# Performance work log

Hardware: AMD Instinct MI355X
Metric: run time of the kernel (lower is better)

## Reference

```python
import jax, jax.numpy as jnp
import numpy as np

B, N, D, C, H = 8, 2048, 768, 2048, 3072
ROPE_BASE = 10000.0


def rms_norm(x, scale, eps=1e-6):
    x32 = x.astype(jnp.float32)
    normed = x32 * jax.lax.rsqrt(jnp.mean(x32 * x32, axis=-1, keepdims=True) + eps)
    return normed.astype(x.dtype) * scale


def apply_rope(x, pos):
    # x: [..., T, D], pos: [..., T] int. Half-split (llama-style) rotary embedding.
    half = x.shape[-1] // 2
    inv_freq = 1.0 / (ROPE_BASE ** (jnp.arange(half, dtype=jnp.float32) / half))
    ang = pos.astype(jnp.float32)[..., None] * inv_freq  # [..., T, half]
    cos, sin = jnp.cos(ang), jnp.sin(ang)
    x1, x2 = x[..., :half], x[..., half:]
    return jnp.concatenate([x1 * cos - x2 * sin, x1 * sin + x2 * cos], axis=-1)


def setup_inputs() -> dict:
    key = jax.random.key(0)
    ks = jax.random.split(key, 12)
    inp = {
        "latents": jax.random.normal(ks[0], (B, N, D), dtype=jnp.float32),
        "tau": jnp.float32(1.0),
        "residual_scaling": jnp.float32(1.0),
        "gumbel_noise_scale": jnp.float32(0.5),
        "positions": jnp.sort(jax.random.randint(ks[1], (B, max(N, C)), 0, 2048), axis=-1),
        # learned parameters (torch Linear weights stored [out, in])
        "codebook": jax.random.normal(ks[2], (C, D), dtype=jnp.float32),
        "norm_context_scale": jnp.ones((D,), jnp.float32),
        "norm_queries_scale": jnp.ones((D,), jnp.float32),
        "norm_ff_scale": jnp.ones((D,), jnp.float32),
        "Wq": jax.random.normal(ks[3], (D, D), jnp.float32) / np.sqrt(D),
        "Wk": jax.random.normal(ks[4], (D, D), jnp.float32) / np.sqrt(D),
        "Wv": jax.random.normal(ks[5], (D, D), jnp.float32) / np.sqrt(D),
        "bv": jnp.zeros((D,), jnp.float32),
        "Wc": jax.random.normal(ks[6], (D, D), jnp.float32) / np.sqrt(D),
        "W1": jax.random.normal(ks[7], (H, D), jnp.float32) / np.sqrt(D),
        "W2": jax.random.normal(ks[8], (D, H), jnp.float32) / np.sqrt(H),
        "W3": jax.random.normal(ks[9], (H, D), jnp.float32) / np.sqrt(D),
    }
    return inp


def reference(latents, tau, residual_scaling, gumbel_noise_scale, positions,
              codebook, norm_context_scale, norm_queries_scale, norm_ff_scale,
              Wq, Wk, Wv, bv, Wc, W1, W2, W3):
    scale = jnp.sqrt(jnp.float32(D))
    normed_context = rms_norm(codebook, norm_context_scale)        # [C, D]
    normed_queries = rms_norm(latents, norm_queries_scale)         # [B, N, D]

    q = jnp.einsum('bnd,ed->bne', normed_queries, Wq)              # [B, N, D]
    k = normed_context @ Wk.T                                      # [C, D]
    v = normed_context @ Wv.T + bv                                 # [C, D]

    q = apply_rope(q, positions[:, :N])                            # [B, N, D]
    k = apply_rope(jnp.broadcast_to(k, (B, C, D)), positions[:, :C])  # [B, C, D]

    log_alpha = jnp.einsum('bnd,bcd->bnc', q, k) / scale           # [B, N, C]

    u = jax.random.uniform(jax.random.key(42), log_alpha.shape, dtype=jnp.float32)
    gumbel = -jnp.log(-jnp.log(u + 1e-10) + 1e-10)
    log_alpha_tau = (log_alpha + gumbel_noise_scale * gumbel) / tau
    z = jax.nn.softmax(log_alpha_tau, axis=-1)                     # [B, N, C]

    attn = jnp.einsum('bnc,cd->bnd', z, v)                         # [B, N, D]
    y = jnp.einsum('bnd,ed->bne', attn, Wc)
    attn_output = residual_scaling * latents + y

    h = rms_norm(attn_output, norm_ff_scale)
    ff = jnp.einsum('bnh,dh->bnd', jax.nn.silu(jnp.einsum('bnd,hd->bnh', h, W1)) * jnp.einsum('bnd,hd->bnh', h, W3), W2)
    codebook_output = attn_output + ff
    return (codebook_output, log_alpha, log_alpha_tau, z)
```

## Files before the change

kernel.cpp:

```cpp
#include <hip/hip_runtime.h>
#include <cstdint>
#include <cstddef>


typedef __bf16 bf16_t;
typedef __bf16 bf16x8 __attribute__((ext_vector_type(8)));
typedef float  f32x4  __attribute__((ext_vector_type(4)));

#define B_    8
#define N_    2048
#define D_    768
#define C_    2048
#define H_    3072
#define NROWS 16384

#define WQ_OFF 0
#define WK_OFF 589824
#define WV_OFF 1179648
#define WC_OFF 1769472
#define W1_OFF 2359296
#define W3_OFF 4718592
#define W2_OFF 7077888
#define WTOT   9437184

#define WS_W     0ull
#define WS_TRIG  18874368ull
#define WS_VCT   25165824ull
#define WS_NC    28311552ull
#define WS_NQ    31457280ull
#define WS_Z     56623104ull
#define WS_H     28311552ull
#define WS_G     157286400ull
#define WS_VB    257949696ull

#define DO_CB    0ull
#define DO_LA    50331648ull
#define DO_LAT   184549376ull
#define DO_Z     318767104ull
#define DO_QBASE 184549376ull
#define DO_KBASE (184549376ull + 50331648ull)
// ... 20 lines not shown
__device__ __forceinline__ void tf_round(uint32_t& x0, uint32_t& x1, int r) {
  x0 += x1; x1 = rotl32(x1, r); x1 ^= x0;
}
__device__ __forceinline__ uint2 threefry2x32(uint32_t k0, uint32_t k1,
                                              uint32_t x0, uint32_t x1) {
  const uint32_t k2 = k0 ^ k1 ^ 0x1BD11BDAu;
  x0 += k0; x1 += k1;
  tf_round(x0,x1,13); tf_round(x0,x1,15); tf_round(x0,x1,26); tf_round(x0,x1,6);
  x0 += k1; x1 += k2 + 1u;
  tf_round(x0,x1,17); tf_round(x0,x1,29); tf_round(x0,x1,16); tf_round(x0,x1,24);
  x0 += k2; x1 += k0 + 2u;
  tf_round(x0,x1,13); tf_round(x0,x1,15); tf_round(x0,x1,26); tf_round(x0,x1,6);
  x0 += k0; x1 += k1 + 3u;
  tf_round(x0,x1,17); tf_round(x0,x1,29); tf_round(x0,x1,16); tf_round(x0,x1,24);
  x0 += k1; x1 += k2 + 4u;
  tf_round(x0,x1,13); tf_round(x0,x1,15); tf_round(x0,x1,26); tf_round(x0,x1,6);
  x0 += k2; x1 += k0 + 5u;
  return make_uint2(x0, x1);
}

#define SWZ(o) ((o) ^ ((((o) >> 7) & 3) << 4))

#define PHASE_MFMA_OPEN() do { \
    block_sync(); \
    asm volatile("s_waitcnt lgkmcnt(0)" ::: "memory"); \
    __builtin_amdgcn_sched_barrier(0); \
    __builtin_amdgcn_s_setprio(1); \
  } while (0)
#define PHASE_MFMA_CLOSE() do { \
    __builtin_amdgcn_s_setprio(0); \
    __builtin_amdgcn_sched_barrier(0); \
  } while (0)

template <int EPI>
__global__ __launch_bounds__(512, 2) void gemm8p(
    const bf16_t* __restrict__ A, const bf16_t* __restrict__ B,
    void* outp, const void* auxp, const float* sptr,
    int M, int N, int K, long sA, long sB, long sO)
{
  __shared__ bf16_t As[2][2][8192];
  __shared__ bf16_t Bs[2][2][8192];
  const int tid  = threadIdx.x;
  const int lane = tid & 63;
  const int wid  = tid >> 6;
  const int wm = wid >> 2, wn = wid & 3;
  const int fr = lane & 15, fg = lane >> 4;
  const int bz = blockIdx.z;
  const bf16_t* Ab = A + (size_t)bz * (size_t)sA;
  const bf16_t* Bb = B + (size_t)bz * (size_t)sB;
  const int tm = blockIdx.y * 256;
  const int tn = blockIdx.x * 256;
  const int nt = K >> 6;

  const bf16_t *srcA0, *srcA1, *srcB0, *srcB1;
  {
    const int d0 = wid * 1024 + lane * 16;
    const int p0 = SWZ(d0);
    srcA0 = Ab + (size_t)(tm + (p0 >> 6)) * K + ((p0 & 63) >> 1);
    srcB0 = Bb + (size_t)(tn + (p0 >> 6)) * K + ((p0 & 63) >> 1);
    const int d1 = 8192 + wid * 1024 + lane * 16;
    const int p1 = SWZ(d1);
    srcA1 = Ab + (size_t)(tm + (p1 >> 6)) * K + ((p1 & 63) >> 1);
    srcB1 = Bb + (size_t)(tn + (p1 >> 6)) * K + ((p1 & 63) >> 1);
  }
  bf16_t* dstA = &As[0][0][0] + wid * 512;
  bf16_t* dstB = &Bs[0][0][0] + wid * 512;

  int olB[4], olA[2][4];
  #pragma unroll
  for (int n = 0; n < 4; ++n) {
    const int o = ((wn * 64 + n * 16 + fr) << 6) + (fg << 4);
    olB[n] = SWZ(o);
  }
  #pragma unroll
  for (int mh = 0; mh < 2; ++mh)
    #pragma unroll
    for (int j = 0; j < 4; ++j) {
      const int o = ((wm * 128 + mh * 64 + j * 16 + fr) << 6) + (fg << 4);
      olA[mh][j] = SWZ(o);
    }

#define STG_A(tile_, kk_) do { \
    const size_t ko_ = (size_t)(tile_) * 64 + (size_t)(kk_) * 32; \
    bf16_t* db_ = dstA + (((tile_) & 1) ? 16384 : 0) + ((kk_) ? 8192 : 0); \
    gl_lds16(srcA0 + ko_, db_); \
    gl_lds16(srcA1 + ko_, db_ + 4096); \
  } while (0)
#define STG_B(tile_, kk_) do { \
    const size_t ko_ = (size_t)(tile_) * 64 + (size_t)(kk_) * 32; \
    bf16_t* db_ = dstB + (((tile_) & 1) ? 16384 : 0) + ((kk_) ? 8192 : 0); \
    gl_lds16(srcB0 + ko_, db_); \
    gl_lds16(srcB1 + ko_, db_ + 4096); \
  } while (0)

  f32x4 acc[8][4] = {};

  STG_A(0, 0); STG_B(0, 0); STG_A(0, 1); STG_B(0, 1);
  STG_B(1, 0); STG_A(1, 0); STG_B(1, 1);
  asm volatile("s_waitcnt vmcnt(6)" ::: "memory");
  block_sync();

  for (int t = 0; t < nt; ++t) {
    const int s = t & 1;
    bf16x8 bfr[4];
    #pragma unroll
    for (int q = 0; q < 4; ++q) {
      const int kk = q >> 1, mh = q & 1;
      if (q == 0)      { if (t + 1 < nt) STG_A(t + 1, 1); }
      else if (q == 1) { if (t + 2 < nt) STG_B(t + 2, 0); }
      else if (q == 2) { if (t + 2 < nt) STG_A(t + 2, 0); }
      else             { if (t + 2 < nt) STG_B(t + 2, 1); }
      if (mh == 0) {
        const char* Bbase = (const char*)&Bs[s][kk][0];
        #pragma unroll
        for (int n = 0; n < 4; ++n)
          bfr[n] = *(const bf16x8*)(Bbase + olB[n]);
      }
      const char* Abase = (const char*)&As[s][kk][0];
      bf16x8 af[4];
      #pragma unroll
      for (int j = 0; j < 4; ++j)
        af[j] = *(const bf16x8*)(Abase + olA[mh][j]);
      PHASE_MFMA_OPEN();
      #pragma unroll
      for (int j = 0; j < 4; ++j) {
        #pragma unroll
        for (int n = 0; n < 4; ++n)
          acc[mh * 4 + j][n] =
            __builtin_amdgcn_mfma_f32_16x16x32_bf16(af[j], bfr[n], acc[mh * 4 + j][n], 0, 0, 0);
      }
      PHASE_MFMA_CLOSE();
      if (q == 3) asm volatile("s_waitcnt vmcnt(6)" ::: "memory");
      block_sync();
    }
  }
#undef STG_A
#undef STG_B

  #pragma unroll
  for (int m = 0; m < 8; ++m) {
    const int rb = wm * 128 + m * 16 + fg * 4;
    #pragma unroll
    for (int n = 0; n < 4; ++n) {
      const int cg = tn + wn * 64 + n * 16 + fr;
      #pragma unroll
      for (int j = 0; j < 4; ++j) {
        const int r = tm + rb + j;
        const float v = acc[m][n][j];
        const size_t idx = (size_t)r * N + cg;
        if (EPI == 1) {
          ((float*)outp)[(size_t)bz * sO + idx] = v * 0.03608439182435161f;
        } else {
          ((float*)outp)[(size_t)bz * sO + idx] = v;
        }
      }
    }
  }
}

template <int EPI>
__global__ __launch_bounds__(512, 2) void gemm_n384(
    const bf16_t* __restrict__ A, const bf16_t* __restrict__ B,
    void* outp, const void* auxp, const float* sptr, int K)
{
  __shared__ bf16_t As[2][2][4096];
  __shared__ bf16_t Bs[2][2][12288];
  const int tid  = threadIdx.x;
  const int lane = tid & 63;
  const int wid  = tid >> 6;
  const int wm = wid >> 2, wn = wid & 3;
  const int fr = lane & 15, fg = lane >> 4;
  const int tm = blockIdx.y * 128;
  const int tn = blockIdx.x * 384;
  const int nt = K >> 6;

  const bf16_t *srcA, *srcB0, *srcB1, *srcB2;
  {
    const int d = wid * 1024 + lane * 16;
    const int p = SWZ(d);
    srcA = A + (size_t)(tm + (p >> 6)) * K + ((p & 63) >> 1);
    srcB0 = B + (size_t)(tn + (p >> 6)) * K + ((p & 63) >> 1);
    const int d1 = 8192 + d, p1 = SWZ(d1);
    srcB1 = B + (size_t)(tn + (p1 >> 6)) * K + ((p1 & 63) >> 1);
    const int d2 = 16384 + d, p2 = SWZ(d2);
    srcB2 = B + (size_t)(tn + (p2 >> 6)) * K + ((p2 & 63) >> 1);
  }
  bf16_t* dstA = &As[0][0][0] + wid * 512;
  bf16_t* dstB = &Bs[0][0][0] + wid * 512;

  int olB[6], olA[2][2];
  #pragma unroll
  for (int n = 0; n < 6; ++n) {
    const int o = ((wn * 96 + n * 16 + fr) << 6) + (fg << 4);
    olB[n] = SWZ(o);
  }
  #pragma unroll
  for (int mh = 0; mh < 2; ++mh)
    #pragma unroll
    for (int j = 0; j < 2; ++j) {
      const int o = ((wm * 64 + (mh * 2 + j) * 16 + fr) << 6) + (fg << 4);
      olA[mh][j] = SWZ(o);
    }

#define STG_A(tile_, kk_) do { \
    const size_t ko_ = (size_t)(tile_) * 64 + (size_t)(kk_) * 32; \
    gl_lds16(srcA + ko_, dstA + (((tile_) & 1) ? 8192 : 0) + ((kk_) ? 4096 : 0)); \
  } while (0)
#define STG_B(tile_, kk_) do { \
    const size_t ko_ = (size_t)(tile_) * 64 + (size_t)(kk_) * 32; \
    bf16_t* db_ = dstB + (((tile_) & 1) ? 24576 : 0) + ((kk_) ? 12288 : 0); \
    gl_lds16(srcB0 + ko_, db_); \
    gl_lds16(srcB1 + ko_, db_ + 4096); \
    gl_lds16(srcB2 + ko_, db_ + 8192); \
  } while (0)

  f32x4 acc[4][6] = {};

  STG_A(0, 0); STG_B(0, 0); STG_A(0, 1); STG_B(0, 1);
  STG_B(1, 0); STG_A(1, 0); STG_B(1, 1);
  asm volatile("s_waitcnt vmcnt(7)" ::: "memory");
  block_sync();

  for (int t = 0; t < nt; ++t) {
    const int s = t & 1;
    bf16x8 bfr[6];
    #pragma unroll
    for (int q = 0; q < 4; ++q) {
      const int kk = q >> 1, mh = q & 1;
      if (q == 0)      { if (t + 1 < nt) STG_A(t + 1, 1); }
      else if (q == 1) { if (t + 2 < nt) STG_B(t + 2, 0); }
      else if (q == 2) { if (t + 2 < nt) STG_A(t + 2, 0); }
      else             { if (t + 2 < nt) STG_B(t + 2, 1); }
      if (mh == 0) {
        const char* Bbase = (const char*)&Bs[s][kk][0];
        #pragma unroll
        for (int n = 0; n < 6; ++n)
          bfr[n] = *(const bf16x8*)(Bbase + olB[n]);
      }
      const char* Abase = (const char*)&As[s][kk][0];
      bf16x8 af[2];
      #pragma unroll
      for (int j = 0; j < 2; ++j)
        af[j] = *(const bf16x8*)(Abase + olA[mh][j]);
      PHASE_MFMA_OPEN();
      #pragma unroll
      for (int j = 0; j < 2; ++j) {
        #pragma unroll
        for (int n = 0; n < 6; ++n)
          acc[mh * 2 + j][n] =
            __builtin_amdgcn_mfma_f32_16x16x32_bf16(af[j], bfr[n], acc[mh * 2 + j][n], 0, 0, 0);
      }
      PHASE_MFMA_CLOSE();
      if (q == 3) asm volatile("s_waitcnt vmcnt(7)" ::: "memory");
      block_sync();
    }
  }
#undef STG_A
#undef STG_B

  const float sval = (EPI == 5) ? sptr[0] : 0.0f;
  #pragma unroll
  for (int m = 0; m < 4; ++m) {
    const int rb = wm * 64 + m * 16 + fg * 4;
    #pragma unroll
    for (int n = 0; n < 6; ++n) {
      const int cg = tn + wn * 96 + n * 16 + fr;
      #pragma unroll
      for (int j = 0; j < 4; ++j) {
        const int r = tm + rb + j;
        const float v = acc[m][n][j];
        const size_t idx = (size_t)r * 768 + cg;
        if (EPI == 2) {
          ((bf16_t*)outp)[idx] = (bf16_t)v;
        } else if (EPI == 5) {
          ((float*)outp)[idx] = sval * ((const float*)auxp)[idx] + v;
        } else {
          ((float*)outp)[idx] = ((const float*)auxp)[idx] + v;
        }
      }
    }
  }
}

__global__ __launch_bounds__(512, 2) void gemm_ff13(
    const bf16_t* __restrict__ A, const bf16_t* __restrict__ B1,
    const bf16_t* __restrict__ B3, bf16_t* __restrict__ G, int K)
{
  __shared__ bf16_t As[2][2][8192];
  __shared__ bf16_t B1s[2][2][4096];
  __shared__ bf16_t B3s[2][2][4096];
  const int tid  = threadIdx.x;
  const int lane = tid & 63;
  const int wid  = tid >> 6;
  const int wm = wid >> 2, wn = wid & 3;
  const int fr = lane & 15, fg = lane >> 4;
  const int tm = blockIdx.y * 256;
  const int tn = blockIdx.x * 128;
  const int nt = K >> 6;

  const bf16_t *srcA0, *srcA1, *srcB1p, *srcB3p;
  {
    const int d0 = wid * 1024 + lane * 16;
    const int p0 = SWZ(d0);
    srcA0 = A + (size_t)(tm + (p0 >> 6)) * K + ((p0 & 63) >> 1);
    srcB1p = B1 + (size_t)(tn + (p0 >> 6)) * K + ((p0 & 63) >> 1);
    srcB3p = B3 + (size_t)(tn + (p0 >> 6)) * K + ((p0 & 63) >> 1);
    const int d1 = 8192 + d0, p1 = SWZ(d1);
    srcA1 = A + (size_t)(tm + (p1 >> 6)) * K + ((p1 & 63) >> 1);
  }
  bf16_t* dstA  = &As[0][0][0]  + wid * 512;
  bf16_t* dstB1 = &B1s[0][0][0] + wid * 512;
  bf16_t* dstB3 = &B3s[0][0][0] + wid * 512;

  int olB[2], olA[2][4];
  #pragma unroll
  for (int n = 0; n < 2; ++n) {
    const int o = ((wn * 32 + n * 16 + fr) << 6) + (fg << 4);
    olB[n] = SWZ(o);
  }
  #pragma unroll
  for (int mh = 0; mh < 2; ++mh)
    #pragma unroll
    for (int j = 0; j < 4; ++j) {
      const int o = ((wm * 128 + mh * 64 + j * 16 + fr) << 6) + (fg << 4);
      olA[mh][j] = SWZ(o);
    }

#define STG_A(tile_, kk_) do { \
    const size_t ko_ = (size_t)(tile_) * 64 + (size_t)(kk_) * 32; \
    bf16_t* db_ = dstA + (((tile_) & 1) ? 16384 : 0) + ((kk_) ? 8192 : 0); \
    gl_lds16(srcA0 + ko_, db_); \
    gl_lds16(srcA1 + ko_, db_ + 4096); \
  } while (0)
#define STG_B(tile_, kk_) do { \
    const size_t ko_ = (size_t)(tile_) * 64 + (size_t)(kk_) * 32; \
    const int ro_ = (((tile_) & 1) ? 8192 : 0) + ((kk_) ? 4096 : 0); \
    gl_lds16(srcB1p + ko_, dstB1 + ro_); \
    gl_lds16(srcB3p + ko_, dstB3 + ro_); \
  } while (0)

  f32x4 acc1[8][2] = {};
  f32x4 acc3[8][2] = {};

  STG_A(0, 0); STG_B(0, 0); STG_A(0, 1); STG_B(0, 1);
  STG_B(1, 0); STG_A(1, 0); STG_B(1, 1);
  asm volatile("s_waitcnt vmcnt(6)" ::: "memory");
  block_sync();

  for (int t = 0; t < nt; ++t) {
    const int s = t & 1;
    bf16x8 b1r[2], b3r[2];
    #pragma unroll
    for (int q = 0; q < 4; ++q) {
      const int kk = q >> 1, mh = q & 1;
      if (q == 0)      { if (t + 1 < nt) STG_A(t + 1, 1); }
      else if (q == 1) { if (t + 2 < nt) STG_B(t + 2, 0); }
      else if (q == 2) { if (t + 2 < nt) STG_A(t + 2, 0); }
      else             { if (t + 2 < nt) STG_B(t + 2, 1); }
      if (mh == 0) {
        const char* B1base = (const char*)&B1s[s][kk][0];
        const char* B3base = (const char*)&B3s[s][kk][0];
        #pragma unroll
        for (int n = 0; n < 2; ++n) {
          b1r[n] = *(const bf16x8*)(B1base + olB[n]);
          b3r[n] = *(const bf16x8*)(B3base + olB[n]);
        }
      }
      const char* Abase = (const char*)&As[s][kk][0];
      bf16x8 af[4];
      #pragma unroll
      for (int j = 0; j < 4; ++j)
        af[j] = *(const bf16x8*)(Abase + olA[mh][j]);
      PHASE_MFMA_OPEN();
      #pragma unroll
      for (int j = 0; j < 4; ++j) {
        #pragma unroll
        for (int n = 0; n < 2; ++n) {
          acc1[mh * 4 + j][n] =
            __builtin_amdgcn_mfma_f32_16x16x32_bf16(af[j], b1r[n], acc1[mh * 4 + j][n], 0, 0, 0);
          acc3[mh * 4 + j][n] =
            __builtin_amdgcn_mfma_f32_16x16x32_bf16(af[j], b3r[n], acc3[mh * 4 + j][n], 0, 0, 0);
        }
      }
      PHASE_MFMA_CLOSE();
      if (q == 3) asm volatile("s_waitcnt vmcnt(6)" ::: "memory");
      block_sync();
    }
  }
#undef STG_A
#undef STG_B

  #pragma unroll
  for (int m = 0; m < 8; ++m) {
    const int rb = wm * 128 + m * 16 + fg * 4;
    #pragma unroll
    for (int n = 0; n < 2; ++n) {
      const int cg = tn + wn * 32 + n * 16 + fr;
      #pragma unroll
      for (int j = 0; j < 4; ++j) {
        const int r = tm + rb + j;
        const float f1 = acc1[m][n][j];
        const float f3 = acc3[m][n][j];
        const float sg = f1 / (1.0f + expf(-f1));
        G[(size_t)r * 3072 + cg] = (bf16_t)(sg * f3);
      }
    }
  }
}

template <int EPI>
__global__ __launch_bounds__(256) void gemm_bt(
    const bf16_t* __restrict__ A, const bf16_t* __restrict__ B,
    void* outp, const void* auxp, int M, int N, int K)
{
  __shared__ bf16_t Asl[128 * 64];
  __shared__ bf16_t Bsl[128 * 64];
  const int tid  = threadIdx.x;
  const int lane = tid & 63;
  const int wid  = tid >> 6;
  const int tm = blockIdx.y * 128;
  const int tn = blockIdx.x * 128;
  const int row0 = (wid & 1) * 64;
  const int col0 = (wid >> 1) * 64;
  const int fr = lane & 15;
  const int fg = lane >> 4;

  f32x4 acc[4][4] = {};

  for (int k0 = 0; k0 < K; k0 += 64) {
    #pragma unroll
    for (int i = 0; i < 4; ++i) {
      const int ebase = (i * 4 + wid) * 512;
      const int e0 = ebase + lane * 8;
      const int r  = e0 >> 6;
      const int c  = e0 & 63;
      gl_lds16(A + (size_t)(tm + r) * K + (k0 + c), &Asl[ebase]);
      gl_lds16(B + (size_t)(tn + r) * K + (k0 + c), &Bsl[ebase]);
    }
    __syncthreads();

    #pragma unroll
    for (int kk = 0; kk < 2; ++kk) {
      bf16x8 af[4], bfv[4];
      #pragma unroll
      for (int m = 0; m < 4; ++m)
        af[m] = *(const bf16x8*)&Asl[(row0 + m * 16 + fr) * 64 + kk * 32 + fg * 8];
      #pragma unroll
      for (int n = 0; n < 4; ++n)
        bfv[n] = *(const bf16x8*)&Bsl[(col0 + n * 16 + fr) * 64 + kk * 32 + fg * 8];
      #pragma unroll
      for (int m = 0; m < 4; ++m) {
        #pragma unroll
        for (int n = 0; n < 4; ++n)
          acc[m][n] = __builtin_amdgcn_mfma_f32_16x16x32_bf16(af[m], bfv[n], acc[m][n], 0, 0, 0);
      }
    }
    __syncthreads();
  }

  #pragma unroll
  for (int m = 0; m < 4; ++m) {
    const int rb = row0 + m * 16 + fg * 4;
    #pragma unroll
    for (int n = 0; n < 4; ++n) {
      const int cg = tn + col0 + n * 16 + fr;
      #pragma unroll
      for (int j = 0; j < 4; ++j) {
        const int r = tm + rb + j;
        const float v = acc[m][n][j];
        if (EPI == 2) {
          ((bf16_t*)outp)[(size_t)r * N + cg] = (bf16_t)v;
        } else if (EPI == 7) {
          ((bf16_t*)outp)[(size_t)cg * M + r] = (bf16_t)v;
        } else if (EPI == 8) {
          ((bf16_t*)outp)[(size_t)r * N + cg] = (bf16_t)(v + ((const float*)auxp)[cg]);
        }
      }
    }
  }
}

__global__ __launch_bounds__(256) void rms_rows(const float* __restrict__ x,
                                                const float* __restrict__ scale,
                                                bf16_t* __restrict__ out)
{
  const int row = blockIdx.x, t = threadIdx.x;
  const float* xr = x + (size_t)row * 768;
  const float v0 = xr[t], v1 = xr[t + 256], v2 = xr[t + 512];
  float ss = v0 * v0 + v1 * v1 + v2 * v2;
  #pragma unroll
  for (int m = 32; m; m >>= 1) ss += __shfl_xor(ss, m);
  __shared__ float red[4];
  if ((t & 63) == 0) red[t >> 6] = ss;
  __syncthreads();
  const float tot = red[0] + red[1] + red[2] + red[3];
  const float inv = rsqrtf(tot / 768.0f + 1e-6f);
  bf16_t* orow = out + (size_t)row * 768;
  orow[t]       = (bf16_t)(v0 * inv * scale[t]);
  orow[t + 256] = (bf16_t)(v1 * inv * scale[t + 256]);
  orow[t + 512] = (bf16_t)(v2 * inv * scale[t + 512]);
}

__global__ __launch_bounds__(128) void trig_fill(float* __restrict__ trig)
{
  const int p = blockIdx.x, t = threadIdx.x;
  #pragma unroll
  for (int j = 0; j < 3; ++j) {
    const int i = t + j * 128;
    const float invf = expf(-(float)i * (9.210340371976184f / 384.0f));
    const float ang  = (float)p * invf;
    trig[(size_t)p * 768 + i]       = cosf(ang);
    trig[(size_t)p * 768 + 384 + i] = sinf(ang);
  }
}

__global__ __launch_bounds__(128) void rope_rows(const bf16_t* __restrict__ src,
                                                 const int* __restrict__ pos,
                                                 const float* __restrict__ trig,
                                                 bf16_t* __restrict__ dst, int mask)
{
  const int row = blockIdx.x, t = threadIdx.x;
  const int p = pos[row];
  const bf16_t* s = src + (size_t)(row & mask) * 768;
  const float* tr = trig + (size_t)p * 768;
  bf16_t* d = dst + (size_t)row * 768;
  #pragma unroll
  for (int j = 0; j < 3; ++j) {
    const int i = t + j * 128;
    const float x1 = (float)s[i], x2 = (float)s[i + 384];
    const float c = tr[i], sn = tr[i + 384];
    d[i]       = (bf16_t)(x1 * c - x2 * sn);
    d[i + 384] = (bf16_t)(x1 * sn + x2 * c);
  }
}

__global__ __launch_bounds__(256) void softmax_g(const float* __restrict__ la,
                                                 float* __restrict__ lat,
                                                 float* __restrict__ z,
                                                 bf16_t* __restrict__ zb,
                                                 const float* __restrict__ taup,
                                                 const float* __restrict__ gnsp)
{
  const int row = blockIdx.x, t = threadIdx.x;
  const float tau = taup[0], gns = gnsp[0];
  const float* lar = la + (size_t)row * 2048;
  float* latr = lat + (size_t)row * 2048;
  float* zr   = z   + (size_t)row * 2048;
  bf16_t* zbr = zb  + (size_t)row * 2048;
  const uint32_t base = (uint32_t)row * 2048u;

  float vals[8];
  float mx = -3.0e38f;
  #pragma unroll
  for (int j = 0; j < 8; ++j) {
    const int c = t + j * 256;
    const uint32_t flat = base + (uint32_t)c;
    const uint2 rr = threefry2x32(0u, 42u, 0u, flat);
    const uint32_t bits = rr.x ^ rr.y;
    const float u = __uint_as_float((bits >> 9) | 0x3f800000u) - 1.0f;
    const float gum = -logf(-logf(u + 1e-10f) + 1e-10f);
    const float v = (lar[c] + gns * gum) / tau;
    vals[j] = v;
    latr[c] = v;
    mx = fmaxf(mx, v);
  }
  #pragma unroll
  for (int m = 32; m; m >>= 1) mx = fmaxf(mx, __shfl_xor(mx, m));
  __shared__ float redm[4];
  if ((t & 63) == 0) redm[t >> 6] = mx;
  __syncthreads();
  mx = fmaxf(fmaxf(redm[0], redm[1]), fmaxf(redm[2], redm[3]));

  float sum = 0.0f;
  #pragma unroll
  for (int j = 0; j < 8; ++j) { vals[j] = expf(vals[j] - mx); sum += vals[j]; }
  #pragma unroll
  for (int m = 32; m; m >>= 1) sum += __shfl_xor(sum, m);
  __shared__ float reds[4];
  if ((t & 63) == 0) reds[t >> 6] = sum;
  __syncthreads();
  sum = reds[0] + reds[1] + reds[2] + reds[3];

  #pragma unroll
  for (int j = 0; j < 8; ++j) {
    const int c = t + j * 256;
    const float zz = vals[j] / sum;
    zr[c]  = zz;
    zbr[c] = (bf16_t)zz;
  }
}

__global__ __launch_bounds__(256) void convert_w(
    const float* __restrict__ wq, const float* __restrict__ wk,
    const float* __restrict__ wv, const float* __restrict__ wc,
    const float* __restrict__ w1, const float* __restrict__ w3,
    const float* __restrict__ w2, bf16_t* __restrict__ dst)
{
  const int idx = blockIdx.x * 256 + threadIdx.x;
  const float* src; int off;
  if      (idx < 589824)  { src = wq; off = 0; }
  else if (idx < 1179648) { src = wk; off = 589824; }
  else if (idx < 1769472) { src = wv; off = 1179648; }
  else if (idx < 2359296) { src = wc; off = 1769472; }
  else if (idx < 4718592) { src = w1; off = 2359296; }
  else if (idx < 7077888) { src = w3; off = 4718592; }
  else                    { src = w2; off = 7077888; }
  dst[idx] = (bf16_t)src[idx - off];
}

extern "C" void kernel_launch(void* const* d_in, const int* in_sizes, int n_in,
                              void* d_out, int out_size, void* d_ws, size_t ws_size,
                              hipStream_t stream)
{
  (void)in_sizes; (void)n_in; (void)out_size; (void)ws_size;
  const float* latents   = (const float*)d_in[0];
  const float* taup      = (const float*)d_in[1];
  const float* rsp       = (const float*)d_in[2];
  const float* gnsp      = (const float*)d_in[3];
  const int*   positions = (const int*)d_in[4];
// ... 3 lines not shown
  const float* nfs       = (const float*)d_in[8];
  const float* Wq = (const float*)d_in[9];
  const float* Wk = (const float*)d_in[10];
  const float* Wv = (const float*)d_in[11];
  const float* bv = (const float*)d_in[12];
  const float* Wc = (const float*)d_in[13];
  const float* W1 = (const float*)d_in[14];
  const float* W2 = (const float*)d_in[15];
  const float* W3 = (const float*)d_in[16];

  char* ws = (char*)d_ws;
  char* ob = (char*)d_out;

  bf16_t* wbf  = (bf16_t*)(ws + WS_W);
  float*  trig = (float*)(ws + WS_TRIG);
  bf16_t* vcT  = (bf16_t*)(ws + WS_VCT);
  bf16_t* nc   = (bf16_t*)(ws + WS_NC);
  bf16_t* nq   = (bf16_t*)(ws + WS_NQ);
  bf16_t* zbuf = (bf16_t*)(ws + WS_Z);
  bf16_t* hbuf = (bf16_t*)(ws + WS_H);
  bf16_t* gbuf = (bf16_t*)(ws + WS_G);
  bf16_t* vbuf = (bf16_t*)(ws + WS_VB);

  float*  out_cb  = (float*)(ob + DO_CB);
  float*  out_la  = (float*)(ob + DO_LA);
  float*  out_lat = (float*)(ob + DO_LAT);
  float*  out_z   = (float*)(ob + DO_Z);
  bf16_t* qbase   = (bf16_t*)(ob + DO_QBASE);
  bf16_t* kbase   = (bf16_t*)(ob + DO_KBASE);
  bf16_t* qrope   = (bf16_t*)(ob + DO_QROPE);
  bf16_t* krope   = (bf16_t*)(ob + DO_KROPE);

  convert_w<<<dim3(WTOT / 256), dim3(256), 0, stream>>>(Wq, Wk, Wv, Wc, W1, W3, W2, wbf);
  rms_rows<<<dim3(C_),    dim3(256), 0, stream>>>(codebook, ncs, nc);
  rms_rows<<<dim3(NROWS), dim3(256), 0, stream>>>(latents,  nqs, nq);
  trig_fill<<<dim3(2048), dim3(128), 0, stream>>>(trig);

  gemm_bt<2><<<dim3(6, 16), dim3(256), 0, stream>>>(nc,   wbf + WK_OFF, kbase, nullptr, C_, D_, D_);
  gemm_bt<8><<<dim3(6, 16), dim3(256), 0, stream>>>(nc,   wbf + WV_OFF, vbuf,  bv,      C_, D_, D_);
  gemm_bt<7><<<dim3(6, 16), dim3(256), 0, stream>>>(vbuf, wbf + WC_OFF, vcT,   nullptr, C_, D_, D_);
  gemm_n384<2><<<dim3(2, 128), dim3(512), 0, stream>>>(nq, wbf + WQ_OFF, qbase, nullptr, nullptr, D_);

  rope_rows<<<dim3(NROWS), dim3(128), 0, stream>>>(qbase, positions, trig, qrope, 0x7fffffff);
  rope_rows<<<dim3(NROWS), dim3(128), 0, stream>>>(kbase, positions, trig, krope, 2047);

  gemm8p<1><<<dim3(8, 8, 8), dim3(512), 0, stream>>>(qrope, krope, out_la, nullptr, nullptr,
                                                     N_, C_, D_, (long)N_ * D_, (long)C_ * D_, (long)N_ * C_);

  softmax_g<<<dim3(NROWS), dim3(256), 0, stream>>>(out_la, out_lat, out_z, zbuf, taup, gnsp);

  gemm_n384<5><<<dim3(2, 128), dim3(512), 0, stream>>>(zbuf, vcT, out_cb, latents, rsp, C_);

  rms_rows<<<dim3(NROWS), dim3(256), 0, stream>>>(out_cb, nfs, hbuf);

  gemm_ff13<<<dim3(24, 64), dim3(512), 0, stream>>>(hbuf, wbf + W1_OFF, wbf + W3_OFF, gbuf, D_);
  gemm_n384<6><<<dim3(2, 128), dim3(512), 0, stream>>>(gbuf, wbf + W2_OFF, out_cb, out_cb, nullptr, H_);
}
```

Measured before the change: 852.6 us.

## Switch GEMMs to 32x32x16 MFMA, fuse RoPE launches, use fast math intrinsics

Moves the three main GEMM kernels from 16x16x32 to 32x32x16 bf16 MFMA tiles, which changes the LDS fragment offsets, the accumulator layout and the epilogue row mapping. The larger MFMA tiles cut the number of LDS fragment reads per FLOP. It also merges the Q and K RoPE launches into one grid, and uses __expf/__logf plus a reciprocal multiply in the softmax and SiLU paths. Fast intrinsics carry small accuracy differences, and the epilogue stores become less coalesced in their row pattern.

```diff
diff --git a/kernel.cpp b/kernel.cpp
--- a/kernel.cpp
+++ b/kernel.cpp
@@ -6,6 +6,7 @@
 typedef __bf16 bf16_t;
 typedef __bf16 bf16x8 __attribute__((ext_vector_type(8)));
 typedef float  f32x4  __attribute__((ext_vector_type(4)));
+typedef float  f32x16 __attribute__((ext_vector_type(16)));
 
 #define B_    8
 #define N_    2048
@@ -92,6 +93,8 @@
     __builtin_amdgcn_sched_barrier(0); \
   } while (0)
 
+#define ROWMAP32(rg, kg) (((rg) & 3) + 8 * ((rg) >> 2) + 4 * (kg))
+
 template <int EPI>
 __global__ __launch_bounds__(512, 2) void gemm8p(
     const bf16_t* __restrict__ A, const bf16_t* __restrict__ B,
@@ -104,7 +107,7 @@
   const int lane = tid & 63;
   const int wid  = tid >> 6;
   const int wm = wid >> 2, wn = wid & 3;
-  const int fr = lane & 15, fg = lane >> 4;
+  const int l31 = lane & 31, kg = lane >> 5;
   const int bz = blockIdx.z;
   const bf16_t* Ab = A + (size_t)bz * (size_t)sA;
   const bf16_t* Bb = B + (size_t)bz * (size_t)sB;
@@ -126,18 +129,20 @@
   bf16_t* dstA = &As[0][0][0] + wid * 512;
   bf16_t* dstB = &Bs[0][0][0] + wid * 512;
 
-  int olB[4], olA[2][4];
-  #pragma unroll
-  for (int n = 0; n < 4; ++n) {
-    const int o = ((wn * 64 + n * 16 + fr) << 6) + (fg << 4);
-    olB[n] = SWZ(o);
-  }
-  #pragma unroll
-  for (int mh = 0; mh < 2; ++mh)
-    #pragma unroll
-    for (int j = 0; j < 4; ++j) {
-      const int o = ((wm * 128 + mh * 64 + j * 16 + fr) << 6) + (fg << 4);
-      olA[mh][j] = SWZ(o);
+  int olA[4][2], olB[2][2];
+  #pragma unroll
+  for (int mb = 0; mb < 4; ++mb)
+    #pragma unroll
+    for (int u = 0; u < 2; ++u) {
+      const int o = ((wm * 128 + mb * 32 + l31) << 6) + u * 32 + (kg << 4);
+      olA[mb][u] = SWZ(o);
+    }
+  #pragma unroll
+  for (int nb = 0; nb < 2; ++nb)
+    #pragma unroll
+    for (int u = 0; u < 2; ++u) {
+      const int o = ((wn * 64 + nb * 32 + l31) << 6) + u * 32 + (kg << 4);
+      olB[nb][u] = SWZ(o);
     }
 
 #define STG_A(tile_, kk_) do { \
@@ -153,7 +158,7 @@
     gl_lds16(srcB1 + ko_, db_ + 4096); \
   } while (0)
 
-  f32x4 acc[8][4] = {};
+  f32x16 acc[4][2] = {};
 
   STG_A(0, 0); STG_B(0, 0); STG_A(0, 1); STG_B(0, 1);
   STG_B(1, 0); STG_A(1, 0); STG_B(1, 1);
@@ -162,7 +167,7 @@
 
   for (int t = 0; t < nt; ++t) {
     const int s = t & 1;
-    bf16x8 bfr[4];
+    bf16x8 bfr[2][2];
     #pragma unroll
     for (int q = 0; q < 4; ++q) {
       const int kk = q >> 1, mh = q & 1;
@@ -173,22 +178,27 @@
       if (mh == 0) {
         const char* Bbase = (const char*)&Bs[s][kk][0];
         #pragma unroll
-        for (int n = 0; n < 4; ++n)
-          bfr[n] = *(const bf16x8*)(Bbase + olB[n]);
+        for (int nb = 0; nb < 2; ++nb)
+          #pragma unroll
+          for (int u = 0; u < 2; ++u)
+            bfr[nb][u] = *(const bf16x8*)(Bbase + olB[nb][u]);
       }
       const char* Abase = (const char*)&As[s][kk][0];
-      bf16x8 af[4];
-      #pragma unroll
-      for (int j = 0; j < 4; ++j)
-        af[j] = *(const bf16x8*)(Abase + olA[mh][j]);
+      bf16x8 af[2][2];
+      #pragma unroll
+      for (int j = 0; j < 2; ++j)
+        #pragma unroll
+        for (int u = 0; u < 2; ++u)
+          af[j][u] = *(const bf16x8*)(Abase + olA[mh * 2 + j][u]);
       PHASE_MFMA_OPEN();
       #pragma unroll
-      for (int j = 0; j < 4; ++j) {
-        #pragma unroll
-        for (int n = 0; n < 4; ++n)
-          acc[mh * 4 + j][n] =
-            __builtin_amdgcn_mfma_f32_16x16x32_bf16(af[j], bfr[n], acc[mh * 4 + j][n], 0, 0, 0);
-      }
+      for (int u = 0; u < 2; ++u)
+        #pragma unroll
+        for (int j = 0; j < 2; ++j)
+          #pragma unroll
+          for (int nb = 0; nb < 2; ++nb)
+            acc[mh * 2 + j][nb] =
+              __builtin_amdgcn_mfma_f32_32x32x16_bf16(af[j][u], bfr[nb][u], acc[mh * 2 + j][nb], 0, 0, 0);
       PHASE_MFMA_CLOSE();
       if (q == 3) asm volatile("s_waitcnt vmcnt(6)" ::: "memory");
       block_sync();
@@ -198,15 +208,14 @@
 #undef STG_B
 
   #pragma unroll
-  for (int m = 0; m < 8; ++m) {
-    const int rb = wm * 128 + m * 16 + fg * 4;
-    #pragma unroll
-    for (int n = 0; n < 4; ++n) {
-      const int cg = tn + wn * 64 + n * 16 + fr;
-      #pragma unroll
-      for (int j = 0; j < 4; ++j) {
-        const int r = tm + rb + j;
-        const float v = acc[m][n][j];
+  for (int mb = 0; mb < 4; ++mb) {
+    #pragma unroll
+    for (int nb = 0; nb < 2; ++nb) {
+      const int cg = tn + wn * 64 + nb * 32 + l31;
+      #pragma unroll
+      for (int rg = 0; rg < 16; ++rg) {
+        const int r = tm + wm * 128 + mb * 32 + ROWMAP32(rg, kg);
+        const float v = acc[mb][nb][rg];
         const size_t idx = (size_t)r * N + cg;
         if (EPI == 1) {
           ((float*)outp)[(size_t)bz * sO + idx] = v * 0.03608439182435161f;
@@ -229,7 +238,7 @@
   const int lane = tid & 63;
   const int wid  = tid >> 6;
   const int wm = wid >> 2, wn = wid & 3;
-  const int fr = lane & 15, fg = lane >> 4;
+  const int l31 = lane & 31, kg = lane >> 5;
   const int tm = blockIdx.y * 128;
   const int tn = blockIdx.x * 384;
   const int nt = K >> 6;
@@ -248,18 +257,20 @@
   bf16_t* dstA = &As[0][0][0] + wid * 512;
   bf16_t* dstB = &Bs[0][0][0] + wid * 512;
 
-  int olB[6], olA[2][2];
-  #pragma unroll
-  for (int n = 0; n < 6; ++n) {
-    const int o = ((wn * 96 + n * 16 + fr) << 6) + (fg << 4);
-    olB[n] = SWZ(o);
-  }
-  #pragma unroll
-  for (int mh = 0; mh < 2; ++mh)
-    #pragma unroll
-    for (int j = 0; j < 2; ++j) {
-      const int o = ((wm * 64 + (mh * 2 + j) * 16 + fr) << 6) + (fg << 4);
-      olA[mh][j] = SWZ(o);
+  int olA[2][2], olB[3][2];
+  #pragma unroll
+  for (int mb = 0; mb < 2; ++mb)
+    #pragma unroll
+    for (int u = 0; u < 2; ++u) {
+      const int o = ((wm * 64 + mb * 32 + l31) << 6) + u * 32 + (kg << 4);
+      olA[mb][u] = SWZ(o);
+    }
+  #pragma unroll
+  for (int nb = 0; nb < 3; ++nb)
+    #pragma unroll
+    for (int u = 0; u < 2; ++u) {
+      const int o = ((wn * 96 + nb * 32 + l31) << 6) + u * 32 + (kg << 4);
+      olB[nb][u] = SWZ(o);
     }
 
 #define STG_A(tile_, kk_) do { \
@@ -274,7 +285,7 @@
     gl_lds16(srcB2 + ko_, db_ + 8192); \
   } while (0)
 
-  f32x4 acc[4][6] = {};
+  f32x16 acc[2][3] = {};
 
   STG_A(0, 0); STG_B(0, 0); STG_A(0, 1); STG_B(0, 1);
   STG_B(1, 0); STG_A(1, 0); STG_B(1, 1);
@@ -283,7 +294,7 @@
 
   for (int t = 0; t < nt; ++t) {
     const int s = t & 1;
-    bf16x8 bfr[6];
+    bf16x8 bfr[3][2];
     #pragma unroll
     for (int q = 0; q < 4; ++q) {
       const int kk = q >> 1, mh = q & 1;
@@ -294,22 +305,23 @@
       if (mh == 0) {
         const char* Bbase = (const char*)&Bs[s][kk][0];
         #pragma unroll
-        for (int n = 0; n < 6; ++n)
-          bfr[n] = *(const bf16x8*)(Bbase + olB[n]);
+        for (int nb = 0; nb < 3; ++nb)
+          #pragma unroll
+          for (int u = 0; u < 2; ++u)
+            bfr[nb][u] = *(const bf16x8*)(Bbase + olB[nb][u]);
       }
       const char* Abase = (const char*)&As[s][kk][0];
       bf16x8 af[2];
       #pragma unroll
-      for (int j = 0; j < 2; ++j)
-        af[j] = *(const bf16x8*)(Abase + olA[mh][j]);
+      for (int u = 0; u < 2; ++u)
+        af[u] = *(const bf16x8*)(Abase + olA[mh][u]);
       PHASE_MFMA_OPEN();
       #pragma unroll
-      for (int j = 0; j < 2; ++j) {
-        #pragma unroll
-        for (int n = 0; n < 6; ++n)
-          acc[mh * 2 + j][n] =
-            __builtin_amdgcn_mfma_f32_16x16x32_bf16(af[j], bfr[n], acc[mh * 2 + j][n], 0, 0, 0);
-      }
+      for (int u = 0; u < 2; ++u)
+        #pragma unroll
+        for (int nb = 0; nb < 3; ++nb)
+          acc[mh][nb] =
+            __builtin_amdgcn_mfma_f32_32x32x16_bf16(af[u], bfr[nb][u], acc[mh][nb], 0, 0, 0);
       PHASE_MFMA_CLOSE();
       if (q == 3) asm volatile("s_waitcnt vmcnt(7)" ::: "memory");
       block_sync();
@@ -320,15 +332,14 @@
 
   const float sval = (EPI == 5) ? sptr[0] : 0.0f;
   #pragma unroll
-  for (int m = 0; m < 4; ++m) {
-    const int rb = wm * 64 + m * 16 + fg * 4;
-    #pragma unroll
-    for (int n = 0; n < 6; ++n) {
-      const int cg = tn + wn * 96 + n * 16 + fr;
-      #pragma unroll
-      for (int j = 0; j < 4; ++j) {
-        const int r = tm + rb + j;
-        const float v = acc[m][n][j];
+  for (int mb = 0; mb < 2; ++mb) {
+    #pragma unroll
+    for (int nb = 0; nb < 3; ++nb) {
+      const int cg = tn + wn * 96 + nb * 32 + l31;
+      #pragma unroll
+      for (int rg = 0; rg < 16; ++rg) {
+        const int r = tm + wm * 64 + mb * 32 + ROWMAP32(rg, kg);
+        const float v = acc[mb][nb][rg];
         const size_t idx = (size_t)r * 768 + cg;
         if (EPI == 2) {
           ((bf16_t*)outp)[idx] = (bf16_t)v;
@@ -353,7 +364,7 @@
   const int lane = tid & 63;
   const int wid  = tid >> 6;
   const int wm = wid >> 2, wn = wid & 3;
-  const int fr = lane & 15, fg = lane >> 4;
+  const int l31 = lane & 31, kg = lane >> 5;
   const int tm = blockIdx.y * 256;
   const int tn = blockIdx.x * 128;
   const int nt = K >> 6;
@@ -372,19 +383,19 @@
   bf16_t* dstB1 = &B1s[0][0][0] + wid * 512;
   bf16_t* dstB3 = &B3s[0][0][0] + wid * 512;
 
-  int olB[2], olA[2][4];
-  #pragma unroll
-  for (int n = 0; n < 2; ++n) {
-    const int o = ((wn * 32 + n * 16 + fr) << 6) + (fg << 4);
-    olB[n] = SWZ(o);
-  }
-  #pragma unroll
-  for (int mh = 0; mh < 2; ++mh)
-    #pragma unroll
-    for (int j = 0; j < 4; ++j) {
-      const int o = ((wm * 128 + mh * 64 + j * 16 + fr) << 6) + (fg << 4);
-      olA[mh][j] = SWZ(o);
-    }
+  int olA[4][2], olB[2];
+  #pragma unroll
+  for (int mb = 0; mb < 4; ++mb)
+    #pragma unroll
+    for (int u = 0; u < 2; ++u) {
+      const int o = ((wm * 128 + mb * 32 + l31) << 6) + u * 32 + (kg << 4);
+      olA[mb][u] = SWZ(o);
+    }
+  #pragma unroll
+  for (int u = 0; u < 2; ++u) {
+    const int o = ((wn * 32 + l31) << 6) + u * 32 + (kg << 4);
+    olB[u] = SWZ(o);
+  }
 
 #define STG_A(tile_, kk_) do { \
     const size_t ko_ = (size_t)(tile_) * 64 + (size_t)(kk_) * 32; \
@@ -399,8 +410,8 @@
     gl_lds16(srcB3p + ko_, dstB3 + ro_); \
   } while (0)
 
-  f32x4 acc1[8][2] = {};
-  f32x4 acc3[8][2] = {};
+  f32x16 acc1[4] = {};
+  f32x16 acc3[4] = {};
 
   STG_A(0, 0); STG_B(0, 0); STG_A(0, 1); STG_B(0, 1);
   STG_B(1, 0); STG_A(1, 0); STG_B(1, 1);
@@ -421,27 +432,28 @@
         const char* B1base = (const char*)&B1s[s][kk][0];
         const char* B3base = (const char*)&B3s[s][kk][0];
         #pragma unroll
-        for (int n = 0; n < 2; ++n) {
-          b1r[n] = *(const bf16x8*)(B1base + olB[n]);
-          b3r[n] = *(const bf16x8*)(B3base + olB[n]);
+        for (int u = 0; u < 2; ++u) {
+          b1r[u] = *(const bf16x8*)(B1base + olB[u]);
+          b3r[u] = *(const bf16x8*)(B3base + olB[u]);
         }
       }
       const char* Abase = (const char*)&As[s][kk][0];
-      bf16x8 af[4];
-      #pragma unroll
-      for (int j = 0; j < 4; ++j)
-        af[j] = *(const bf16x8*)(Abase + olA[mh][j]);
+      bf16x8 af[2][2];
+      #pragma unroll
+      for (int j = 0; j < 2; ++j)
+        #pragma unroll
+        for (int u = 0; u < 2; ++u)
+          af[j][u] = *(const bf16x8*)(Abase + olA[mh * 2 + j][u]);
       PHASE_MFMA_OPEN();
       #pragma unroll
-      for (int j = 0; j < 4; ++j) {
-        #pragma unroll
-        for (int n = 0; n < 2; ++n) {
-          acc1[mh * 4 + j][n] =
-            __builtin_amdgcn_mfma_f32_16x16x32_bf16(af[j], b1r[n], acc1[mh * 4 + j][n], 0, 0, 0);
-          acc3[mh * 4 + j][n] =
-            __builtin_amdgcn_mfma_f32_16x16x32_bf16(af[j], b3r[n], acc3[mh * 4 + j][n], 0, 0, 0);
+      for (int u = 0; u < 2; ++u)
+        #pragma unroll
+        for (int j = 0; j < 2; ++j) {
+          acc1[mh * 2 + j] =
+            __builtin_amdgcn_mfma_f32_32x32x16_bf16(af[j][u], b1r[u], acc1[mh * 2 + j], 0, 0, 0);
+          acc3[mh * 2 + j] =
+            __builtin_amdgcn_mfma_f32_32x32x16_bf16(af[j][u], b3r[u], acc3[mh * 2 + j], 0, 0, 0);
         }
-      }
       PHASE_MFMA_CLOSE();
       if (q == 3) asm volatile("s_waitcnt vmcnt(6)" ::: "memory");
       block_sync();
@@ -451,19 +463,15 @@
 #undef STG_B
 
   #pragma unroll
-  for (int m = 0; m < 8; ++m) {
-    const int rb = wm * 128 + m * 16 + fg * 4;
-    #pragma unroll
-    for (int n = 0; n < 2; ++n) {
-      const int cg = tn + wn * 32 + n * 16 + fr;
-      #pragma unroll
-      for (int j = 0; j < 4; ++j) {
-        const int r = tm + rb + j;
-        const float f1 = acc1[m][n][j];
-        const float f3 = acc3[m][n][j];
-        const float sg = f1 / (1.0f + expf(-f1));
-        G[(size_t)r * 3072 + cg] = (bf16_t)(sg * f3);
-      }
+  for (int mb = 0; mb < 4; ++mb) {
+    const int cg = tn + wn * 32 + l31;
+    #pragma unroll
+    for (int rg = 0; rg < 16; ++rg) {
+      const int r = tm + wm * 128 + mb * 32 + ROWMAP32(rg, kg);
+      const float f1 = acc1[mb][rg];
+      const float f3 = acc3[mb][rg];
+      const float sg = f1 / (1.0f + __expf(-f1));
+      G[(size_t)r * 3072 + cg] = (bf16_t)(sg * f3);
     }
   }
 }
@@ -574,16 +582,28 @@
   }
 }
 
-__global__ __launch_bounds__(128) void rope_rows(const bf16_t* __restrict__ src,
-                                                 const int* __restrict__ pos,
-                                                 const float* __restrict__ trig,
-                                                 bf16_t* __restrict__ dst, int mask)
-{
-  const int row = blockIdx.x, t = threadIdx.x;
-  const int p = pos[row];
-  const bf16_t* s = src + (size_t)(row & mask) * 768;
+__global__ __launch_bounds__(128) void rope_qk(const bf16_t* __restrict__ qsrc,
+                                               const bf16_t* __restrict__ ksrc,
+                                               const int* __restrict__ pos,
+                                               const float* __restrict__ trig,
+                                               bf16_t* __restrict__ qdst,
+                                               bf16_t* __restrict__ kdst)
+{
+  const int bid = blockIdx.x, t = threadIdx.x;
+  const bf16_t* s;
+  bf16_t* d;
+  int p;
+  if (bid < NROWS) {
+    p = pos[bid];
+    s = qsrc + (size_t)bid * 768;
+    d = qdst + (size_t)bid * 768;
+  } else {
+    const int row = bid - NROWS;
+    p = pos[row];
+    s = ksrc + (size_t)(row & 2047) * 768;
+    d = kdst + (size_t)row * 768;
+  }
   const float* tr = trig + (size_t)p * 768;
-  bf16_t* d = dst + (size_t)row * 768;
   #pragma unroll
   for (int j = 0; j < 3; ++j) {
     const int i = t + j * 128;
@@ -618,7 +638,7 @@
     const uint2 rr = threefry2x32(0u, 42u, 0u, flat);
     const uint32_t bits = rr.x ^ rr.y;
     const float u = __uint_as_float((bits >> 9) | 0x3f800000u) - 1.0f;
-    const float gum = -logf(-logf(u + 1e-10f) + 1e-10f);
+    const float gum = -__logf(-__logf(u + 1e-10f) + 1e-10f);
     const float v = (lar[c] + gns * gum) / tau;
     vals[j] = v;
     latr[c] = v;
@@ -633,7 +653,7 @@
 
   float sum = 0.0f;
   #pragma unroll
-  for (int j = 0; j < 8; ++j) { vals[j] = expf(vals[j] - mx); sum += vals[j]; }
+  for (int j = 0; j < 8; ++j) { vals[j] = __expf(vals[j] - mx); sum += vals[j]; }
   #pragma unroll
   for (int m = 32; m; m >>= 1) sum += __shfl_xor(sum, m);
   __shared__ float reds[4];
@@ -641,10 +661,11 @@
   __syncthreads();
   sum = reds[0] + reds[1] + reds[2] + reds[3];
 
+  const float rinv = 1.0f / sum;
   #pragma unroll
   for (int j = 0; j < 8; ++j) {
     const int c = t + j * 256;
-    const float zz = vals[j] / sum;
+    const float zz = vals[j] * rinv;
     zr[c]  = zz;
     zbr[c] = (bf16_t)zz;
   }
@@ -723,8 +744,7 @@
   gemm_bt<7><<<dim3(6, 16), dim3(256), 0, stream>>>(vbuf, wbf + WC_OFF, vcT,   nullptr, C_, D_, D_);
   gemm_n384<2><<<dim3(2, 128), dim3(512), 0, stream>>>(nq, wbf + WQ_OFF, qbase, nullptr, nullptr, D_);
 
-  rope_rows<<<dim3(NROWS), dim3(128), 0, stream>>>(qbase, positions, trig, qrope, 0x7fffffff);
-  rope_rows<<<dim3(NROWS), dim3(128), 0, stream>>>(kbase, positions, trig, krope, 2047);
+  rope_qk<<<dim3(2 * NROWS), dim3(128), 0, stream>>>(qbase, kbase, positions, trig, qrope, krope);
 
   gemm8p<1><<<dim3(8, 8, 8), dim3(512), 0, stream>>>(qrope, krope, out_la, nullptr, nullptr,
                                                      N_, C_, D_, (long)N_ * D_, (long)C_ * D_, (long)N_ * C_);
```

New measurement: 846.7 us. Within noise of the previous version (-0.7%).

## Swizzle GEMM block order for XCDs, fuse K/V, RMS and RoPE launches, use fast math

Applied to the files above, without the earlier changes.

Remaps linear block IDs in the three big GEMMs so consecutive blocks on each of the eight XCDs work on neighbouring tiles, aiming for better L2 reuse. It merges the K and V projections into one kernel that shares the A tile, and merges the two RMS-norm launches and the two RoPE launches into single kernels. It also swaps expf and logf for their fast intrinsics in SwiGLU, Gumbel and softmax, and replaces the per-element divide with a reciprocal multiply. Fast math may shift Gumbel and softmax outputs slightly.

```diff
diff --git a/kernel.cpp b/kernel.cpp
--- a/kernel.cpp
+++ b/kernel.cpp
@@ -105,11 +105,17 @@
   const int wid  = tid >> 6;
   const int wm = wid >> 2, wn = wid & 3;
   const int fr = lane & 15, fg = lane >> 4;
-  const int bz = blockIdx.z;
+
+  const int lin = (blockIdx.z * gridDim.y + blockIdx.y) * gridDim.x + blockIdx.x;
+  const int swzb = (lin & 7) * 64 + (lin >> 3);
+  const int bz = swzb >> 6;
+  const int ny = (swzb & 63) >> 3;
+  const int nx = swzb & 7;
+
   const bf16_t* Ab = A + (size_t)bz * (size_t)sA;
   const bf16_t* Bb = B + (size_t)bz * (size_t)sB;
-  const int tm = blockIdx.y * 256;
-  const int tn = blockIdx.x * 256;
+  const int tm = ny * 256;
+  const int tn = nx * 256;
   const int nt = K >> 6;
 
   const bf16_t *srcA0, *srcA1, *srcB0, *srcB1;
@@ -230,8 +236,14 @@
   const int wid  = tid >> 6;
   const int wm = wid >> 2, wn = wid & 3;
   const int fr = lane & 15, fg = lane >> 4;
-  const int tm = blockIdx.y * 128;
-  const int tn = blockIdx.x * 384;
+
+  const int lin = blockIdx.y * 2 + blockIdx.x;
+  const int swzb = (lin & 7) * 32 + (lin >> 3);
+  const int ny = swzb >> 1;
+  const int nx = swzb & 1;
+
+  const int tm = ny * 128;
+  const int tn = nx * 384;
   const int nt = K >> 6;
 
   const bf16_t *srcA, *srcB0, *srcB1, *srcB2;
@@ -354,8 +366,18 @@
   const int wid  = tid >> 6;
   const int wm = wid >> 2, wn = wid & 3;
   const int fr = lane & 15, fg = lane >> 4;
-  const int tm = blockIdx.y * 256;
-  const int tn = blockIdx.x * 128;
+
+  const int lin = blockIdx.y * 24 + blockIdx.x;
+  const int swzb = (lin & 7) * 192 + (lin >> 3);
+  const int cj = swzb / 192;
+  const int local = swzb - cj * 192;
+  const int st = local / 24;
+  const int rr = local - st * 24;
+  const int nx = cj * 3 + (rr % 3);
+  const int ny = st * 8 + (rr / 3);
+
+  const int tm = ny * 256;
+  const int tn = nx * 128;
   const int nt = K >> 6;
 
   const bf16_t *srcA0, *srcA1, *srcB1p, *srcB3p;
@@ -461,8 +483,82 @@
         const int r = tm + rb + j;
         const float f1 = acc1[m][n][j];
         const float f3 = acc3[m][n][j];
-        const float sg = f1 / (1.0f + expf(-f1));
+        const float sg = f1 / (1.0f + __expf(-f1));
         G[(size_t)r * 3072 + cg] = (bf16_t)(sg * f3);
+      }
+    }
+  }
+}
+
+__global__ __launch_bounds__(256) void gemm_kv(
+    const bf16_t* __restrict__ A, const bf16_t* __restrict__ Bk,
+    const bf16_t* __restrict__ Bv, bf16_t* __restrict__ kout,
+    bf16_t* __restrict__ vout, const float* __restrict__ bias,
+    int M, int N, int K)
+{
+  __shared__ bf16_t Asl[128 * 64];
+  __shared__ bf16_t Bks[128 * 64];
+  __shared__ bf16_t Bvs[128 * 64];
+  const int tid  = threadIdx.x;
+  const int lane = tid & 63;
+  const int wid  = tid >> 6;
+  const int tm = blockIdx.y * 128;
+  const int tn = blockIdx.x * 128;
+  const int row0 = (wid & 1) * 64;
+  const int col0 = (wid >> 1) * 64;
+  const int fr = lane & 15;
+  const int fg = lane >> 4;
+
+  f32x4 acck[4][4] = {};
+  f32x4 accv[4][4] = {};
+
+  for (int k0 = 0; k0 < K; k0 += 64) {
+    #pragma unroll
+    for (int i = 0; i < 4; ++i) {
+      const int ebase = (i * 4 + wid) * 512;
+      const int e0 = ebase + lane * 8;
+      const int r  = e0 >> 6;
+      const int c  = e0 & 63;
+      gl_lds16(A  + (size_t)(tm + r) * K + (k0 + c), &Asl[ebase]);
+      gl_lds16(Bk + (size_t)(tn + r) * K + (k0 + c), &Bks[ebase]);
+      gl_lds16(Bv + (size_t)(tn + r) * K + (k0 + c), &Bvs[ebase]);
+    }
+    __syncthreads();
+
+    #pragma unroll
+    for (int kk = 0; kk < 2; ++kk) {
+      bf16x8 af[4], bk[4], bv2[4];
+      #pragma unroll
+      for (int m = 0; m < 4; ++m)
+        af[m] = *(const bf16x8*)&Asl[(row0 + m * 16 + fr) * 64 + kk * 32 + fg * 8];
+      #pragma unroll
+      for (int n = 0; n < 4; ++n) {
+        bk[n]  = *(const bf16x8*)&Bks[(col0 + n * 16 + fr) * 64 + kk * 32 + fg * 8];
+        bv2[n] = *(const bf16x8*)&Bvs[(col0 + n * 16 + fr) * 64 + kk * 32 + fg * 8];
+      }
+      #pragma unroll
+      for (int m = 0; m < 4; ++m) {
+        #pragma unroll
+        for (int n = 0; n < 4; ++n) {
+          acck[m][n] = __builtin_amdgcn_mfma_f32_16x16x32_bf16(af[m], bk[n],  acck[m][n], 0, 0, 0);
+          accv[m][n] = __builtin_amdgcn_mfma_f32_16x16x32_bf16(af[m], bv2[n], accv[m][n], 0, 0, 0);
+        }
+      }
+    }
+    __syncthreads();
+  }
+
+  #pragma unroll
+  for (int m = 0; m < 4; ++m) {
+    const int rb = row0 + m * 16 + fg * 4;
+    #pragma unroll
+    for (int n = 0; n < 4; ++n) {
+      const int cg = tn + col0 + n * 16 + fr;
+      #pragma unroll
+      for (int j = 0; j < 4; ++j) {
+        const int r = tm + rb + j;
+        kout[(size_t)r * N + cg] = (bf16_t)acck[m][n][j];
+        vout[(size_t)r * N + cg] = (bf16_t)(accv[m][n][j] + bias[cg]);
       }
     }
   }
@@ -528,16 +624,43 @@
       for (int j = 0; j < 4; ++j) {
         const int r = tm + rb + j;
         const float v = acc[m][n][j];
-        if (EPI == 2) {
+        if (EPI == 7) {
+          ((bf16_t*)outp)[(size_t)cg * M + r] = (bf16_t)v;
+        } else {
           ((bf16_t*)outp)[(size_t)r * N + cg] = (bf16_t)v;
-        } else if (EPI == 7) {
-          ((bf16_t*)outp)[(size_t)cg * M + r] = (bf16_t)v;
-        } else if (EPI == 8) {
-          ((bf16_t*)outp)[(size_t)r * N + cg] = (bf16_t)(v + ((const float*)auxp)[cg]);
         }
       }
     }
   }
+}
+
+__global__ __launch_bounds__(256) void rms_all(
+    const float* __restrict__ cb, const float* __restrict__ lt,
+    const float* __restrict__ ncs, const float* __restrict__ nqs,
+    bf16_t* __restrict__ nc, bf16_t* __restrict__ nq)
+{
+  const int row = blockIdx.x, t = threadIdx.x;
+  const float* xr;
+  const float* scale;
+  bf16_t* orow;
+  if (row < 2048) {
+    xr = cb + (size_t)row * 768; scale = ncs; orow = nc + (size_t)row * 768;
+  } else {
+    const int r2 = row - 2048;
+    xr = lt + (size_t)r2 * 768; scale = nqs; orow = nq + (size_t)r2 * 768;
+  }
+  const float v0 = xr[t], v1 = xr[t + 256], v2 = xr[t + 512];
+  float ss = v0 * v0 + v1 * v1 + v2 * v2;
+  #pragma unroll
+  for (int m = 32; m; m >>= 1) ss += __shfl_xor(ss, m);
+  __shared__ float red[4];
+  if ((t & 63) == 0) red[t >> 6] = ss;
+  __syncthreads();
+  const float tot = red[0] + red[1] + red[2] + red[3];
+  const float inv = rsqrtf(tot / 768.0f + 1e-6f);
+  orow[t]       = (bf16_t)(v0 * inv * scale[t]);
+  orow[t + 256] = (bf16_t)(v1 * inv * scale[t + 256]);
+  orow[t + 512] = (bf16_t)(v2 * inv * scale[t + 512]);
 }
 
 __global__ __launch_bounds__(256) void rms_rows(const float* __restrict__ x,
@@ -574,16 +697,28 @@
   }
 }
 
-__global__ __launch_bounds__(128) void rope_rows(const bf16_t* __restrict__ src,
-                                                 const int* __restrict__ pos,
-                                                 const float* __restrict__ trig,
-                                                 bf16_t* __restrict__ dst, int mask)
-{
-  const int row = blockIdx.x, t = threadIdx.x;
-  const int p = pos[row];
-  const bf16_t* s = src + (size_t)(row & mask) * 768;
+__global__ __launch_bounds__(128) void rope_qk(const bf16_t* __restrict__ qsrc,
+                                               const bf16_t* __restrict__ ksrc,
+                                               const int* __restrict__ pos,
+                                               const float* __restrict__ trig,
+                                               bf16_t* __restrict__ qdst,
+                                               bf16_t* __restrict__ kdst)
+{
+  const int bid = blockIdx.x, t = threadIdx.x;
+  const bf16_t* s;
+  bf16_t* d;
+  int p;
+  if (bid < NROWS) {
+    p = pos[bid];
+    s = qsrc + (size_t)bid * 768;
+    d = qdst + (size_t)bid * 768;
+  } else {
+    const int row = bid - NROWS;
+    p = pos[row];
+    s = ksrc + (size_t)(row & 2047) * 768;
+    d = kdst + (size_t)row * 768;
+  }
   const float* tr = trig + (size_t)p * 768;
-  bf16_t* d = dst + (size_t)row * 768;
   #pragma unroll
   for (int j = 0; j < 3; ++j) {
     const int i = t + j * 128;
@@ -618,7 +753,7 @@
     const uint2 rr = threefry2x32(0u, 42u, 0u, flat);
     const uint32_t bits = rr.x ^ rr.y;
     const float u = __uint_as_float((bits >> 9) | 0x3f800000u) - 1.0f;
-    const float gum = -logf(-logf(u + 1e-10f) + 1e-10f);
+    const float gum = -__logf(-__logf(u + 1e-10f) + 1e-10f);
     const float v = (lar[c] + gns * gum) / tau;
     vals[j] = v;
     latr[c] = v;
@@ -633,7 +768,7 @@
 
   float sum = 0.0f;
   #pragma unroll
-  for (int j = 0; j < 8; ++j) { vals[j] = expf(vals[j] - mx); sum += vals[j]; }
+  for (int j = 0; j < 8; ++j) { vals[j] = __expf(vals[j] - mx); sum += vals[j]; }
   #pragma unroll
   for (int m = 32; m; m >>= 1) sum += __shfl_xor(sum, m);
   __shared__ float reds[4];
@@ -641,10 +776,11 @@
   __syncthreads();
   sum = reds[0] + reds[1] + reds[2] + reds[3];
 
+  const float rinv = 1.0f / sum;
   #pragma unroll
   for (int j = 0; j < 8; ++j) {
     const int c = t + j * 256;
-    const float zz = vals[j] / sum;
+    const float zz = vals[j] * rinv;
     zr[c]  = zz;
     zbr[c] = (bf16_t)zz;
   }
@@ -714,17 +850,15 @@
   bf16_t* krope   = (bf16_t*)(ob + DO_KROPE);
 
   convert_w<<<dim3(WTOT / 256), dim3(256), 0, stream>>>(Wq, Wk, Wv, Wc, W1, W3, W2, wbf);
-  rms_rows<<<dim3(C_),    dim3(256), 0, stream>>>(codebook, ncs, nc);
-  rms_rows<<<dim3(NROWS), dim3(256), 0, stream>>>(latents,  nqs, nq);
+  rms_all<<<dim3(C_ + NROWS), dim3(256), 0, stream>>>(codebook, latents, ncs, nqs, nc, nq);
   trig_fill<<<dim3(2048), dim3(128), 0, stream>>>(trig);
 
-  gemm_bt<2><<<dim3(6, 16), dim3(256), 0, stream>>>(nc,   wbf + WK_OFF, kbase, nullptr, C_, D_, D_);
-  gemm_bt<8><<<dim3(6, 16), dim3(256), 0, stream>>>(nc,   wbf + WV_OFF, vbuf,  bv,      C_, D_, D_);
-  gemm_bt<7><<<dim3(6, 16), dim3(256), 0, stream>>>(vbuf, wbf + WC_OFF, vcT,   nullptr, C_, D_, D_);
+  gemm_kv<<<dim3(6, 16), dim3(256), 0, stream>>>(nc, wbf + WK_OFF, wbf + WV_OFF,
+                                                 kbase, vbuf, bv, C_, D_, D_);
+  gemm_bt<7><<<dim3(6, 16), dim3(256), 0, stream>>>(vbuf, wbf + WC_OFF, vcT, nullptr, C_, D_, D_);
   gemm_n384<2><<<dim3(2, 128), dim3(512), 0, stream>>>(nq, wbf + WQ_OFF, qbase, nullptr, nullptr, D_);
 
-  rope_rows<<<dim3(NROWS), dim3(128), 0, stream>>>(qbase, positions, trig, qrope, 0x7fffffff);
-  rope_rows<<<dim3(NROWS), dim3(128), 0, stream>>>(kbase, positions, trig, krope, 2047);
+  rope_qk<<<dim3(2 * NROWS), dim3(128), 0, stream>>>(qbase, kbase, positions, trig, qrope, krope);
 
   gemm8p<1><<<dim3(8, 8, 8), dim3(512), 0, stream>>>(qrope, krope, out_la, nullptr, nullptr,
                                                      N_, C_, D_, (long)N_ * D_, (long)C_ * D_, (long)N_ * C_);
```

Measured after the change: 796.1 us (median of 2 runs). 1.07x faster.
